# Optimization experiments

Measured on AMD Instinct MI355X. Metric: run time of the kernel, lower is better.

## Reference

```python
import jax, jax.numpy as jnp
import numpy as np

B, S, H = 2, 2048, 1024          # batch, seq, hidden_size
I = 512                          # expert_ffn_hidden_size
E_R, E_Z = 32, 8                 # routed experts, zero (identity) experts
E_T = E_R + E_Z                  # total experts
K = 6                            # moe_topk
SCALE = 2.5                      # routed_scaling_factor
W_INIT = 0.02


def setup_inputs() -> dict:
    key = jax.random.key(0)
    k0, k1, k2, k3 = jax.random.split(key, 4)
    return {
        "hidden_states": jax.random.normal(k0, (B, S, H), jnp.float32),
        "classifier_weight": jax.random.normal(k1, (E_T, H), jnp.float32) * W_INIT,
        "e_score_correction_bias": jnp.zeros((E_T,), jnp.float32),
        "gate_up_proj": jax.random.normal(k2, (E_T, 2 * I, H), jnp.float32) * W_INIT,
        "down_proj": jax.random.normal(k3, (E_R, H, I), jnp.float32) * W_INIT,
    }


def reference(hidden_states, classifier_weight, e_score_correction_bias,
              gate_up_proj, down_proj):
    orig_shape = hidden_states.shape
    x = hidden_states.reshape(-1, H).astype(jnp.float32)      # [T, H]
    T = x.shape[0]

    # ---- router (fp32 like the torch code) ----
    logits = x @ classifier_weight.T                          # [T, E_T]
    scores = jax.nn.softmax(logits, axis=-1)
    _, topk_idx = jax.lax.top_k(scores + e_score_correction_bias[None, :], K)
    topk_w = jnp.take_along_axis(scores, topk_idx, axis=1) * SCALE  # [T, K]

    # dense per-(token, expert) combine weights; 0 for unselected experts
    w_full = jnp.zeros((T, E_T), jnp.float32).at[
        jnp.arange(T)[:, None], topk_idx].add(topk_w)          # [T, E_T]

    # zero experts: weighted identity
    zero_w = w_full[:, E_R:].sum(axis=-1, keepdims=True)       # [T, 1]
    out0 = x * zero_w

    # routed experts: SwiGLU MLP per expert, scanned over experts
    routed_w = w_full[:, :E_R].T                               # [E_R, T]

    def body(out, xs):
        Wgu, Wd, we = xs                                       # [2I,H],[H,I],[T]
        gate, up = jnp.split(x @ Wgu.T, 2, axis=-1)            # [T, I] each
        y = (jax.nn.silu(gate) * up) @ Wd.T                    # [T, H]
        return out + we[:, None] * y, None

    out, _ = jax.lax.scan(body, out0, (gate_up_proj[:E_R], down_proj, routed_w))
    return out.reshape(orig_shape).astype(hidden_states.dtype)
```

## Files before the change

### kernel.cpp

```cpp
#include <hip/hip_runtime.h>
#include <float.h>
#include <math.h>

#define TT 4096
#define HH 1024
#define II 512
#define E_R 32
#define E_T 40
#define TOPK 6
#define SCALE_F 2.5f
#define MAXTILES 224

typedef __bf16 bf16x8 __attribute__((ext_vector_type(8)));
typedef float f32x4 __attribute__((ext_vector_type(4)));

__device__ inline unsigned short f2bf(float f) {
  __bf16 h = (__bf16)f;
  return __builtin_bit_cast(unsigned short, h);
}

__device__ inline bf16x8 cvt8v(float4 a, float4 b) {
  bf16x8 v;
  v[0] = (__bf16)a.x; v[1] = (__bf16)a.y; v[2] = (__bf16)a.z; v[3] = (__bf16)a.w;
  v[4] = (__bf16)b.x; v[5] = (__bf16)b.y; v[6] = (__bf16)b.z; v[7] = (__bf16)b.w;
  return v;
}

__device__ inline void gload_lds16(const void* g, void* l) {
  __builtin_amdgcn_global_load_lds(
      (__attribute__((address_space(1))) void*)g,
      (__attribute__((address_space(3))) void*)l, 16, 0, 0);
}

__device__ inline bf16x8 lds_frag(const unsigned short* base, int row, int kb) {
  int byte = (row * 128 + kb * 2) ^ ((row & 7) << 4);
  uint4 v = *reinterpret_cast<const uint4*>(reinterpret_cast<const char*>(base) + byte);
  return __builtin_bit_cast(bf16x8, v);
}

__device__ inline bf16x8 lds_frag_f32(const float* base, int row, int kb) {
  int key = row & 15;
  int c0 = (kb >> 2) ^ key;
  int c1 = ((kb >> 2) + 1) ^ key;
  const char* p = reinterpret_cast<const char*>(base) + row * 256;
  float4 lo = *reinterpret_cast<const float4*>(p + c0 * 16);
  float4 hi = *reinterpret_cast<const float4*>(p + c1 * 16);
  return cvt8v(lo, hi);
}

__device__ inline f32x4 mfma16(bf16x8 a, bf16x8 b, f32x4 c) {
  return __builtin_amdgcn_mfma_f32_16x16x32_bf16(a, b, c, 0, 0, 0);
}

__global__ __launch_bounds__(256) void k_logits(const float* __restrict__ x,
                                                const float* __restrict__ wcls,
                                                float* __restrict__ logits,
                                                unsigned short* __restrict__ xb,
                                                int* __restrict__ counts,
                                                int* __restrict__ ticket) {
  __shared__ float4 ws4[E_T * 64];
  const int tid = threadIdx.x;
  const int lane = tid & 63;
  const int wave = tid >> 6;
  const int token = blockIdx.x * 4 + wave;
  if (blockIdx.x == 0) {
    if (tid < E_R) counts[tid] = 0;
    else if (tid == E_R) *ticket = 0;
  }
  const float4* x4 = reinterpret_cast<const float4*>(x);
  const float4* w4 = reinterpret_cast<const float4*>(wcls);

  float acc[E_T];
  #pragma unroll
  for (int e = 0; e < E_T; ++e) acc[e] = 0.f;

  for (int c = 0; c < 4; ++c) {
    if (c) __syncthreads();
    #pragma unroll
    for (int j = 0; j < 10; ++j) {
      int v = tid + j * 256;
      int e = v >> 6, kq = v & 63;
      ws4[v] = w4[e * 256 + c * 64 + kq];
    }
    float4 xv = x4[(size_t)token * 256 + c * 64 + lane];
    ushort4 s;
    s.x = f2bf(xv.x); s.y = f2bf(xv.y); s.z = f2bf(xv.z); s.w = f2bf(xv.w);
    reinterpret_cast<ushort4*>(xb + (size_t)token * HH)[c * 64 + lane] = s;
    __syncthreads();
    #pragma unroll
    for (int e = 0; e < E_T; ++e) {
      float4 w = ws4[e * 64 + lane];
      acc[e] += xv.x * w.x + xv.y * w.y + xv.z * w.z + xv.w * w.w;
    }
  }

  float mine = 0.f;
  #pragma unroll
  for (int e = 0; e < E_T; ++e) {
    float r = acc[e];
    #pragma unroll
    for (int o = 32; o; o >>= 1) r += __shfl_xor(r, o);
    if (lane == e) mine = r;
  }
  if (lane < E_T) logits[(size_t)token * E_T + lane] = mine;
}

__global__ __launch_bounds__(256) void k_topk(
    const float* __restrict__ logits, const float* __restrict__ bias,
    const float* __restrict__ x, int* __restrict__ counts,
    int* __restrict__ tok_list, float* __restrict__ wt_list,
    float* __restrict__ out,
    int* __restrict__ offsets, int* __restrict__ tiles, int* __restrict__ ticket) {
  __shared__ float s_zw[64];
  const int tid = threadIdx.x;
  if (tid < 64) {
    int t = blockIdx.x * 64 + tid;
    float l[E_T];
    const float4* lp = reinterpret_cast<const float4*>(logits + (size_t)t * E_T);
    #pragma unroll
    for (int j = 0; j < E_T / 4; ++j) {
      float4 v = lp[j];
      l[j * 4 + 0] = v.x; l[j * 4 + 1] = v.y; l[j * 4 + 2] = v.z; l[j * 4 + 3] = v.w;
    }
    float m = -FLT_MAX;
    #pragma unroll
    for (int e = 0; e < E_T; ++e) m = fmaxf(m, l[e]);
    float den = 0.f;
    #pragma unroll
    for (int e = 0; e < E_T; ++e) { l[e] = __expf(l[e] - m); den += l[e]; }
    float inv = 1.f / den;
    float sel[E_T];
    #pragma unroll
    for (int e = 0; e < E_T; ++e) { l[e] *= inv; sel[e] = l[e] + bias[e]; }

    unsigned long long used = 0ull;
    float zw = 0.f;
    for (int k = 0; k < TOPK; ++k) {
      float bv = -FLT_MAX; int bj = 0;
      #pragma unroll
      for (int e = 0; e < E_T; ++e) {
        float v = ((used >> e) & 1ull) ? -FLT_MAX : sel[e];
        if (v > bv) { bv = v; bj = e; }
      }
      used |= 1ull << bj;
      float wgt = (bv - bias[bj]) * SCALE_F;
      if (bj >= E_R) {
        zw += wgt;
      } else {
        int p = atomicAdd(&counts[bj], 1);
        tok_list[bj * TT + p] = t;
        wt_list[bj * TT + p] = wgt;
      }
    }
    s_zw[tid] = zw;
  }
  __syncthreads();

  const float4* x4 = reinterpret_cast<const float4*>(x) + (size_t)blockIdx.x * 64 * 256;
  float4* o4 = reinterpret_cast<float4*>(out) + (size_t)blockIdx.x * 64 * 256;
  #pragma unroll
  for (int j = 0; j < 64; ++j) {
    int i = tid + j * 256;
    float zw = s_zw[i >> 8];
    float4 v = x4[i];
    v.x *= zw; v.y *= zw; v.z *= zw; v.w *= zw;
    o4[i] = v;
  }

  __threadfence();
  __syncthreads();
  if (tid == 0) {
    int tk = atomicAdd(ticket, 1);
    if (tk == (int)gridDim.x - 1) {
      int s = 0, idx = 0;
      for (int e = 0; e < E_R; ++e) {
        int c = atomicAdd(&counts[e], 0);
        offsets[e] = s;
        s += c;
        for (int r0 = 0; r0 < c; r0 += 128) tiles[1 + idx++] = (e << 16) | r0;
      }
      offsets[E_R] = s;
      tiles[0] = idx;
    }
  }
}

__global__ __launch_bounds__(256, 3) void k_gemm1(
    const unsigned short* __restrict__ xb, const float* __restrict__ gup,
    const int* __restrict__ tok_list, const int* __restrict__ counts,
    const int* __restrict__ offsets, const int* __restrict__ tiles,
    unsigned short* __restrict__ inter) {
  const int nt = tiles[0];
  if ((int)blockIdx.y >= nt) return;
  const int tv = tiles[1 + blockIdx.y];
  const int e = tv >> 16;
  const int row0 = tv & 0xffff;
  const int cnt = counts[e];
  const int off = offsets[e];
  const int n0 = blockIdx.x * 64;
  const int tid = threadIdx.x;
  const int lane = tid & 63;
  const int wave = tid >> 6;
  const int wr = wave >> 1;
  const int wc = wave & 1;

  __shared__ __align__(16) unsigned short lA[128 * 64];
  __shared__ __align__(16) float lBg[64 * 64];
  __shared__ __align__(16) float lBu[64 * 64];
  __shared__ int toks[128];

  if (tid < 128) {
    int r = row0 + tid;
    toks[tid] = tok_list[e * TT + (r < cnt ? r : cnt - 1)];
  }
  __syncthreads();

  unsigned aoff[4];
  #pragma unroll
  for (int i = 0; i < 4; ++i) {
    int lrow = wave * 32 + i * 8 + (lane >> 3);
    aoff[i] = (unsigned)toks[lrow] * HH + (((lane & 7) ^ (lrow & 7)) * 8);
  }
  const float* gbase = gup + (size_t)e * 1024 * HH;
  unsigned boff[4];
  #pragma unroll
  for (int i = 0; i < 4; ++i) {
    int rt = wave * 16 + i * 4 + (lane >> 4);
    boff[i] = (unsigned)(n0 + rt) * HH + (((lane & 15) ^ (rt & 15)) * 4);
  }
  const unsigned upjump = 512u * HH;

  f32x4 accg[4][2] = {}; f32x4 accu[4][2] = {};

  for (int k0 = 0; k0 < HH; k0 += 64) {
    #pragma unroll
    for (int i = 0; i < 4; ++i)
      gload_lds16(xb + aoff[i] + k0, lA + (wave * 32 + i * 8) * 64);
    #pragma unroll
    for (int i = 0; i < 4; ++i) {
      gload_lds16(gbase + boff[i] + k0,          lBg + (wave * 16 + i * 4) * 64);
      gload_lds16(gbase + boff[i] + upjump + k0, lBu + (wave * 16 + i * 4) * 64);
    }
    __syncthreads();
    #pragma unroll
    for (int ks = 0; ks < 2; ++ks) {
      int kb = ks * 32 + ((lane >> 4) << 3);
      bf16x8 a[4], g[2], u[2];
      #pragma unroll
      for (int i = 0; i < 4; ++i) a[i] = lds_frag(lA, wr * 64 + i * 16 + (lane & 15), kb);
      #pragma unroll
      for (int j = 0; j < 2; ++j) {
        g[j] = lds_frag_f32(lBg, wc * 32 + j * 16 + (lane & 15), kb);
        u[j] = lds_frag_f32(lBu, wc * 32 + j * 16 + (lane & 15), kb);
      }
      #pragma unroll
      for (int i = 0; i < 4; ++i)
        #pragma unroll
        for (int j = 0; j < 2; ++j) {
          accg[i][j] = mfma16(a[i], g[j], accg[i][j]);
          accu[i][j] = mfma16(a[i], u[j], accu[i][j]);
        }
    }
    __syncthreads();
  }

  #pragma unroll
  for (int i = 0; i < 4; ++i)
    #pragma unroll
    for (int j = 0; j < 2; ++j)
      #pragma unroll
      for (int r = 0; r < 4; ++r) {
        int rloc = wr * 64 + i * 16 + ((lane >> 4) << 2) + r;
        int grow = row0 + rloc;
        if (grow < cnt) {
          int col = n0 + wc * 32 + j * 16 + (lane & 15);
          float gv = accg[i][j][r], uv = accu[i][j][r];
          float act = gv / (1.f + __expf(-gv)) * uv;
          inter[(size_t)(off + grow) * II + col] = f2bf(act);
        }
      }
}

__global__ __launch_bounds__(256, 3) void k_gemm2(
    const unsigned short* __restrict__ inter, const float* __restrict__ dwn,
    const int* __restrict__ tok_list, const float* __restrict__ wt_list,
    const int* __restrict__ counts, const int* __restrict__ offsets,
    const int* __restrict__ tiles, float* __restrict__ out) {
  const int nt = tiles[0];
  if ((int)blockIdx.y >= nt) return;
  const int tv = tiles[1 + blockIdx.y];
  const int e = tv >> 16;
  const int row0 = tv & 0xffff;
  const int cnt = counts[e];
  const int off = offsets[e];
  const int h0 = blockIdx.x * 128;
  const int tid = threadIdx.x;
  const int lane = tid & 63;
  const int wave = tid >> 6;
  const int wr = wave >> 1;
  const int wc = wave & 1;

  __shared__ __align__(16) unsigned short lA[128 * 64];
  __shared__ __align__(16) float lB[128 * 64];
  __shared__ int toks[128];
  __shared__ float wts[128];

  if (tid < 128) {
    int r = row0 + tid;
    int rc = r < cnt ? r : cnt - 1;
    toks[tid] = tok_list[e * TT + rc];
    wts[tid] = (r < cnt) ? wt_list[e * TT + rc] : 0.f;
  }
  __syncthreads();

  unsigned aoff[4];
  #pragma unroll
  for (int i = 0; i < 4; ++i) {
    int lrow = wave * 32 + i * 8 + (lane >> 3);
    int rr = row0 + lrow; rr = rr < cnt ? rr : cnt - 1;
    aoff[i] = (unsigned)(off + rr) * II + (((lane & 7) ^ (lrow & 7)) * 8);
  }
  const float* dbase = dwn + (size_t)e * HH * II;
  unsigned boff[8];
  #pragma unroll
  for (int i = 0; i < 8; ++i) {
    int rt = wave * 32 + i * 4 + (lane >> 4);
    boff[i] = (unsigned)(h0 + rt) * II + (((lane & 15) ^ (rt & 15)) * 4);
  }

  f32x4 acc[4][4] = {};

  for (int k0 = 0; k0 < II; k0 += 64) {
    #pragma unroll
    for (int i = 0; i < 4; ++i)
      gload_lds16(inter + aoff[i] + k0, lA + (wave * 32 + i * 8) * 64);
    #pragma unroll
    for (int i = 0; i < 8; ++i)
      gload_lds16(dbase + boff[i] + k0, lB + (wave * 32 + i * 4) * 64);
    __syncthreads();
    #pragma unroll
    for (int ks = 0; ks < 2; ++ks) {
      int kb = ks * 32 + ((lane >> 4) << 3);
      bf16x8 a[4], b[4];
      #pragma unroll
      for (int i = 0; i < 4; ++i) a[i] = lds_frag(lA, wr * 64 + i * 16 + (lane & 15), kb);
      #pragma unroll
      for (int j = 0; j < 4; ++j) b[j] = lds_frag_f32(lB, wc * 64 + j * 16 + (lane & 15), kb);
      #pragma unroll
      for (int i = 0; i < 4; ++i)
        #pragma unroll
        for (int j = 0; j < 4; ++j)
          acc[i][j] = mfma16(a[i], b[j], acc[i][j]);
    }
    __syncthreads();
  }

  #pragma unroll
  for (int i = 0; i < 4; ++i)
    #pragma unroll
    for (int j = 0; j < 4; ++j)
      #pragma unroll
      for (int r = 0; r < 4; ++r) {
        int rloc = wr * 64 + i * 16 + ((lane >> 4) << 2) + r;
        int grow = row0 + rloc;
        if (grow < cnt) {
          int h = h0 + wc * 64 + j * 16 + (lane & 15);
          unsafeAtomicAdd(&out[(size_t)toks[rloc] * HH + h], acc[i][j][r] * wts[rloc]);
        }
      }
}


extern "C" void kernel_launch(void* const* d_in, const int* in_sizes, int n_in,
                              void* d_out, int out_size, void* d_ws, size_t ws_size,
                              hipStream_t stream) {
  const float* x    = (const float*)d_in[0];
  const float* wcls = (const float*)d_in[1];
  const float* bias = (const float*)d_in[2];
  const float* gup  = (const float*)d_in[3];
  const float* dwn  = (const float*)d_in[4];
  float* out = (float*)d_out;

  char* w = (char*)d_ws;
  unsigned short* xb    = (unsigned short*)(w + 0);
  int* counts           = (int*)(w + 8388608);
  int* offsets          = (int*)(w + 8388736);
  int* ticket           = (int*)(w + 8388736 + 160);
  int* tok_list         = (int*)(w + 8388992);
  float* wt_list        = (float*)(w + 8913280);
  float* logits         = (float*)(w + 9437568);
  int* tiles            = (int*)(w + 10092928);
  unsigned short* inter = (unsigned short*)(w + 10097024);

  k_logits<<<1024, 256, 0, stream>>>(x, wcls, logits, xb, counts, ticket);
  k_topk<<<64, 256, 0, stream>>>(logits, bias, x, counts, tok_list, wt_list,
                                 out, offsets, tiles, ticket);
  k_gemm1<<<dim3(8, MAXTILES), 256, 0, stream>>>(xb, gup, tok_list, counts, offsets, tiles, inter);
  k_gemm2<<<dim3(8, MAXTILES), 256, 0, stream>>>(inter, dwn, tok_list, wt_list, counts,
                                                 offsets, tiles, out);
}
```

Before: 259.1 us.

## Replace atomic scatter in down-proj GEMM with bf16 staging and per-token combine

```diff
diff --git a/kernel.cpp b/kernel.cpp
--- a/kernel.cpp
+++ b/kernel.cpp
@@ -108,8 +108,9 @@
 __global__ __launch_bounds__(256) void k_topk(
     const float* __restrict__ logits, const float* __restrict__ bias,
     const float* __restrict__ x, int* __restrict__ counts,
-    int* __restrict__ tok_list, float* __restrict__ wt_list,
-    float* __restrict__ out,
+    int* __restrict__ tok_list,
+    int* __restrict__ route_ep, float* __restrict__ route_w,
+    int* __restrict__ route_n, float* __restrict__ out,
     int* __restrict__ offsets, int* __restrict__ tiles, int* __restrict__ ticket) {
   __shared__ float s_zw[64];
   const int tid = threadIdx.x;
@@ -135,6 +136,7 @@
 
     unsigned long long used = 0ull;
     float zw = 0.f;
+    int nr = 0;
     for (int k = 0; k < TOPK; ++k) {
       float bv = -FLT_MAX; int bj = 0;
       #pragma unroll
@@ -149,10 +151,13 @@
       } else {
         int p = atomicAdd(&counts[bj], 1);
         tok_list[bj * TT + p] = t;
-        wt_list[bj * TT + p] = wgt;
+        route_ep[t * TOPK + nr] = (bj << 16) | p;
+        route_w[t * TOPK + nr] = wgt;
+        nr++;
       }
     }
     s_zw[tid] = zw;
+    route_n[t] = nr;
   }
   __syncthreads();
 
@@ -283,9 +288,8 @@
 
 __global__ __launch_bounds__(256, 3) void k_gemm2(
     const unsigned short* __restrict__ inter, const float* __restrict__ dwn,
-    const int* __restrict__ tok_list, const float* __restrict__ wt_list,
     const int* __restrict__ counts, const int* __restrict__ offsets,
-    const int* __restrict__ tiles, float* __restrict__ out) {
+    const int* __restrict__ tiles, unsigned short* __restrict__ inter2) {
   const int nt = tiles[0];
   if ((int)blockIdx.y >= nt) return;
   const int tv = tiles[1 + blockIdx.y];
@@ -302,16 +306,6 @@
 
   __shared__ __align__(16) unsigned short lA[128 * 64];
   __shared__ __align__(16) float lB[128 * 64];
-  __shared__ int toks[128];
-  __shared__ float wts[128];
-
-  if (tid < 128) {
-    int r = row0 + tid;
-    int rc = r < cnt ? r : cnt - 1;
-    toks[tid] = tok_list[e * TT + rc];
-    wts[tid] = (r < cnt) ? wt_list[e * TT + rc] : 0.f;
-  }
-  __syncthreads();
 
   unsigned aoff[4];
   #pragma unroll
@@ -365,9 +359,30 @@
         int grow = row0 + rloc;
         if (grow < cnt) {
           int h = h0 + wc * 64 + j * 16 + (lane & 15);
-          unsafeAtomicAdd(&out[(size_t)toks[rloc] * HH + h], acc[i][j][r] * wts[rloc]);
+          inter2[(size_t)(off + grow) * HH + h] = f2bf(acc[i][j][r]);
         }
       }
+}
+
+__global__ __launch_bounds__(256) void k_combine(
+    const int* __restrict__ offsets, const int* __restrict__ route_ep,
+    const float* __restrict__ route_w, const int* __restrict__ route_n,
+    const unsigned short* __restrict__ inter2, float* __restrict__ out) {
+  const int t = blockIdx.x;
+  const int tid = threadIdx.x;
+  const int n = route_n[t];
+  float4 o = reinterpret_cast<const float4*>(out)[t * 256 + tid];
+  for (int i = 0; i < n; ++i) {
+    int ep = route_ep[t * TOPK + i];
+    int row = offsets[ep >> 16] + (ep & 0xffff);
+    float w = route_w[t * TOPK + i];
+    ushort4 v = reinterpret_cast<const ushort4*>(inter2 + (size_t)row * HH)[tid];
+    o.x += w * __builtin_bit_cast(float, (unsigned)v.x << 16);
+    o.y += w * __builtin_bit_cast(float, (unsigned)v.y << 16);
+    o.z += w * __builtin_bit_cast(float, (unsigned)v.z << 16);
+    o.w += w * __builtin_bit_cast(float, (unsigned)v.w << 16);
+  }
+  reinterpret_cast<float4*>(out)[t * 256 + tid] = o;
 }
 
 
@@ -387,15 +402,18 @@
   int* offsets          = (int*)(w + 8388736);
   int* ticket           = (int*)(w + 8388736 + 160);
   int* tok_list         = (int*)(w + 8388992);
-  float* wt_list        = (float*)(w + 8913280);
-  float* logits         = (float*)(w + 9437568);
-  int* tiles            = (int*)(w + 10092928);
-  unsigned short* inter = (unsigned short*)(w + 10097024);
+  float* logits         = (float*)(w + 8913280);
+  int* tiles            = (int*)(w + 9568640);
+  int* route_ep         = (int*)(w + 9572736);
+  float* route_w        = (float*)(w + 9671040);
+  int* route_n          = (int*)(w + 9769344);
+  unsigned short* inter = (unsigned short*)(w + 9785728);
+  unsigned short* inter2 = (unsigned short*)(w + 34951552);
 
   k_logits<<<1024, 256, 0, stream>>>(x, wcls, logits, xb, counts, ticket);
-  k_topk<<<64, 256, 0, stream>>>(logits, bias, x, counts, tok_list, wt_list,
-                                 out, offsets, tiles, ticket);
+  k_topk<<<64, 256, 0, stream>>>(logits, bias, x, counts, tok_list,
+                                 route_ep, route_w, route_n, out, offsets, tiles, ticket);
   k_gemm1<<<dim3(8, MAXTILES), 256, 0, stream>>>(xb, gup, tok_list, counts, offsets, tiles, inter);
-  k_gemm2<<<dim3(8, MAXTILES), 256, 0, stream>>>(inter, dwn, tok_list, wt_list, counts,
-                                                 offsets, tiles, out);
-}
+  k_gemm2<<<dim3(8, MAXTILES), 256, 0, stream>>>(inter, dwn, counts, offsets, tiles, inter2);
+  k_combine<<<TT, 256, 0, stream>>>(offsets, route_ep, route_w, route_n, inter2, out);
+}
```

After: 240.0 us. 7.4% less time.
